# Optimization experiments

Hardware: AMD Instinct MI355X
Metric: run time of the kernel (lower is better)

## Reference

```python
import jax, jax.numpy as jnp
import numpy as np

DIM = 1024
HEADS = 16
SCALE = DIM ** -0.5  # note: source scales by full dim, not head dim


def setup_inputs() -> dict:
    key = jax.random.key(0)
    k1, k2, k3 = jax.random.split(key, 3)
    b, n = 2, 2048
    x = jax.random.normal(k1, (b, n, DIM), dtype=jnp.float32)
    w_qkv = jax.random.normal(k2, (3 * DIM, DIM), dtype=jnp.float32) * (DIM ** -0.5)
    w_out = jax.random.normal(k3, (DIM, DIM), dtype=jnp.float32) * (DIM ** -0.5)
    b_out = jnp.zeros((DIM,), dtype=jnp.float32)
    return {"x": x, "w_qkv": w_qkv, "w_out": w_out, "b_out": b_out}


def reference(x, w_qkv, w_out, b_out):
    b, n, d = x.shape
    h = HEADS
    hd = d // h
    # torch Linear: y = x @ W.T
    qkv = x @ w_qkv.T  # [b, n, 3d]
    q, k, v = jnp.split(qkv, 3, axis=-1)
    # reshape to [b, h, n, hd]
    def to_heads(t):
        return t.reshape(b, n, h, hd).transpose(0, 2, 1, 3)
    q, k, v = to_heads(q), to_heads(k), to_heads(v)
    dots = jnp.einsum('bhqd,bhkd->bhqk', q, k) * SCALE
    attn = jax.nn.softmax(dots, axis=-1)
    out = jnp.einsum('bhqk,bhkd->bhqd', attn, v)
    out = out.transpose(0, 2, 1, 3).reshape(b, n, d)
    return out @ w_out.T + b_out
```

## Files before the change

kernel.cpp:

```cpp
#include <hip/hip_runtime.h>

typedef __attribute__((ext_vector_type(8))) _Float16 half8;
typedef __attribute__((ext_vector_type(4))) _Float16 half4;
typedef __attribute__((ext_vector_type(2))) __fp16 fp16x2;
typedef __attribute__((ext_vector_type(4))) float f32x4;
typedef __attribute__((ext_vector_type(4))) unsigned int u32x4;
typedef __attribute__((ext_vector_type(2))) unsigned int u32x2;

#define NSEQ 2048
#define DIMM 1024
#define NH   16
#define HD   64

typedef const void __attribute__((address_space(1))) gvoid_t;
typedef void __attribute__((address_space(3))) svoid_t;

__device__ __forceinline__ void gload_lds16(const void* g, void* l) {
  __builtin_amdgcn_global_load_lds((gvoid_t*)g, (svoid_t*)l, 16, 0, 0);
}

union H2U { fp16x2 h; unsigned int u; };

__global__ __launch_bounds__(256) void cvt_all(const float* __restrict__ x,
                                               const float* __restrict__ wqkv,
                                               const float* __restrict__ wout,
                                               _Float16* __restrict__ xh,
                                               _Float16* __restrict__ wqkvh,
                                               _Float16* __restrict__ wouth) {
  int i = blockIdx.x * 256 + threadIdx.x;
  const float* src;
  _Float16* dst;
  int off;
  if (i < 524288) { src = x; dst = xh; off = i; }
  else if (i < 917504) { src = wqkv; dst = wqkvh; off = i - 524288; }
  else { src = wout; dst = wouth; off = i - 917504; }
  const float4* p = (const float4*)src + (size_t)off * 2;
  float4 v0 = p[0], v1 = p[1];
  half8 h;
  h[0] = (_Float16)v0.x; h[1] = (_Float16)v0.y; h[2] = (_Float16)v0.z; h[3] = (_Float16)v0.w;
  h[4] = (_Float16)v1.x; h[5] = (_Float16)v1.y; h[6] = (_Float16)v1.z; h[7] = (_Float16)v1.w;
  *((half8*)dst + off) = h;
}

__device__ __forceinline__ void gemm_mainloop(const _Float16* __restrict__ A,
                                              const _Float16* __restrict__ B,
                                              int am0, int bn0,
                                              _Float16* As, _Float16* Bs,
                                              f32x4 acc[4][4]) {
  const int tid = threadIdx.x;
  const int w = tid >> 6, lane = tid & 63;
  const int lr = lane >> 2;
  const int lc = (lane & 3) * 8;
  const int wm = (w >> 1) * 64, wn = (w & 1) * 64;
  const int g = lane >> 4, ln = lane & 15;

  for (int k0 = 0; k0 < 1024; k0 += 32) {
#pragma unroll
    for (int rr = 0; rr < 4; ++rr) {
      int c = rr * 4 + w;
      if (c < 8) {
        gload_lds16(A + (size_t)(am0 + c * 16 + lr) * 1024 + k0 + lc, As + c * 512);
      } else {
        int cb = c - 8;
        gload_lds16(B + (size_t)(bn0 + cb * 16 + lr) * 1024 + k0 + lc, Bs + cb * 512);
      }
    }
    __syncthreads();
    half8 af[4], bf[4];
#pragma unroll
    for (int mi = 0; mi < 4; ++mi)
      af[mi] = *(const half8*)(As + (wm + mi * 16 + ln) * 32 + g * 8);
#pragma unroll
    for (int ni = 0; ni < 4; ++ni)
      bf[ni] = *(const half8*)(Bs + (wn + ni * 16 + ln) * 32 + g * 8);
#pragma unroll
    for (int mi = 0; mi < 4; ++mi)
#pragma unroll
      for (int ni = 0; ni < 4; ++ni)
        acc[mi][ni] = __builtin_amdgcn_mfma_f32_16x16x32_f16(af[mi], bf[ni], acc[mi][ni], 0, 0, 0);
    __syncthreads();
  }
}

union SmemQKV {
  struct { _Float16 a[128 * 32]; _Float16 b[128 * 32]; } ab;
  _Float16 t[128 * 136];
};

#define QSCALE 0.0450843450f

__global__ __launch_bounds__(256) void gemm_qkv(const _Float16* __restrict__ x,
                                                const _Float16* __restrict__ wqkv,
                                                _Float16* __restrict__ qh,
                                                _Float16* __restrict__ kh,
                                                _Float16* __restrict__ vt) {
  __shared__ SmemQKV sh;
  f32x4 acc[4][4];
#pragma unroll
  for (int i = 0; i < 4; ++i)
#pragma unroll
    for (int j = 0; j < 4; ++j) acc[i][j] = (f32x4){0.f, 0.f, 0.f, 0.f};
  const int bm = blockIdx.x, bn = blockIdx.y;
  gemm_mainloop(x, wqkv, bm * 128, bn * 128, sh.ab.a, sh.ab.b, acc);

  const int tid = threadIdx.x;
  const int w = tid >> 6, lane = tid & 63;
  const int g = lane >> 4, ln = lane & 15;
  const int wm = (w >> 1) * 64, wn = (w & 1) * 64;
  const int sec = bn >> 3;
  const int cbase = (bn & 7) * 128;

  if (sec < 2) {
    _Float16* dst = (sec == 0) ? qh : kh;
    const float scale = (sec == 0) ? QSCALE : 1.0f;
#pragma unroll
    for (int mi = 0; mi < 4; ++mi) {
      int row = bm * 128 + wm + mi * 16 + g * 4;
      int bidx = row >> 11, nidx = row & 2047;
#pragma unroll
      for (int ni = 0; ni < 4; ++ni) {
        int col = cbase + wn + ni * 16 + ln;
        int h = col >> 6, d = col & 63;
        _Float16* p = dst + ((size_t)(bidx * NH + h) * NSEQ + nidx) * HD + d;
#pragma unroll
        for (int r = 0; r < 4; ++r) p[r * HD] = (_Float16)(acc[mi][ni][r] * scale);
      }
    }
  } else {
    __syncthreads();
#pragma unroll
    for (int mi = 0; mi < 4; ++mi)
#pragma unroll
      for (int ni = 0; ni < 4; ++ni)
#pragma unroll
        for (int r = 0; r < 4; ++r)
          sh.t[(wn + ni * 16 + ln) * 136 + wm + mi * 16 + g * 4 + r] = (_Float16)acc[mi][ni][r];
    __syncthreads();
    const int row0 = bm * 128;
    const int bidx = row0 >> 11, n0 = row0 & 2047;
#pragma unroll
    for (int i = 0; i < 8; ++i) {
      int ci = i * 256 + tid;
      int drow = ci >> 4, nofs = (ci & 15) * 8;
      int col = cbase + drow;
      int h = col >> 6, d = col & 63;
      u32x4 val = *(const u32x4*)(sh.t + drow * 136 + nofs);
      *(u32x4*)(vt + ((size_t)(bidx * NH + h) * HD + d) * NSEQ + n0 + nofs) = val;
    }
  }
}

__global__ __launch_bounds__(512, 1) void attn_fwd(const _Float16* __restrict__ qg,
                                                   const _Float16* __restrict__ kg,
                                                   const _Float16* __restrict__ vg,
                                                   _Float16* __restrict__ ao) {
  __shared__ _Float16 Ks[2][64 * 64];
  __shared__ _Float16 Vs[2][64 * 64];
  __shared__ _Float16 Ps[8][32 * 64];

  const int bid = blockIdx.x;
  const int swz = (bid & 7) * 32 + (bid >> 3);
  const int bh = swz >> 3, qt = swz & 7;
  const int tid = threadIdx.x, w = tid >> 6, lane = tid & 63;
  const int g = lane >> 4, ln = lane & 15;
  const int sw8 = ln & 7;

  const _Float16* qp = qg + (size_t)bh * NSEQ * HD;
  const _Float16* kp = kg + (size_t)bh * NSEQ * HD;
  const _Float16* vp = vg + (size_t)bh * HD * NSEQ;
  char* psw = (char*)&Ps[w][0];

  const int qr = qt * 256 + w * 32;

  half8 qf[2][2];
#pragma unroll
  for (int qb = 0; qb < 2; ++qb)
#pragma unroll
    for (int dk = 0; dk < 2; ++dk)
      qf[qb][dk] = *(const half8*)(qp + (size_t)(qr + qb * 16 + ln) * HD + dk * 32 + g * 8);
  asm volatile("" ::: "memory");

  const int rsub = lane >> 3;
  const int csw = ((lane & 7) ^ rsub) << 3;

#define STAGE(buf, tt)                                                              \
  {                                                                                 \
    gload_lds16(kp + (size_t)(tt) * 64 * HD + (size_t)(w * 8 + rsub) * HD + csw,    \
                &Ks[buf][w * 512]);                                                 \
    gload_lds16(vp + (size_t)(w * 8 + rsub) * NSEQ + (tt) * 64 + csw,               \
                &Vs[buf][w * 512]);                                                 \
  }

  STAGE(0, 0);

  float lsum[2] = {0.f, 0.f};
  f32x4 oacc[4][2];
#pragma unroll
  for (int sd = 0; sd < 4; ++sd)
#pragma unroll
    for (int qb = 0; qb < 2; ++qb) oacc[sd][qb] = (f32x4){0.f, 0.f, 0.f, 0.f};
  const f32x4 fz = (f32x4){0.f, 0.f, 0.f, 0.f};

#define TILE_BODY(cur)                                                              \
  {                                                                                 \
    f32x4 sacc[4][2];                                                               \
    __builtin_amdgcn_s_setprio(1);                                                  \
    _Pragma("unroll")                                                               \
    for (int s = 0; s < 4; ++s) {                                                   \
      const _Float16* kb = &Ks[cur][(s * 16 + ln) * 64];                            \
      half8 kf0 = *(const half8*)(kb + ((g ^ sw8) << 3));                           \
      half8 kf1 = *(const half8*)(kb + (((4 + g) ^ sw8) << 3));                     \
      sacc[s][0] = __builtin_amdgcn_mfma_f32_16x16x32_f16(kf0, qf[0][0], fz, 0, 0, 0);            \
      sacc[s][0] = __builtin_amdgcn_mfma_f32_16x16x32_f16(kf1, qf[0][1], sacc[s][0], 0, 0, 0);    \
      sacc[s][1] = __builtin_amdgcn_mfma_f32_16x16x32_f16(kf0, qf[1][0], fz, 0, 0, 0);            \
      sacc[s][1] = __builtin_amdgcn_mfma_f32_16x16x32_f16(kf1, qf[1][1], sacc[s][1], 0, 0, 0);    \
    }                                                                               \
    __builtin_amdgcn_s_setprio(0);                                                  \
    _Pragma("unroll")                                                               \
    for (int qb = 0; qb < 2; ++qb) {                                                \
      const int q = qb * 16 + ln;                                                   \
      float rs = 0.f;                                                               \
      _Pragma("unroll")                                                             \
      for (int s = 0; s < 4; ++s) {                                                 \
        float e0 = __builtin_amdgcn_exp2f(sacc[s][qb][0]);                          \
        float e1 = __builtin_amdgcn_exp2f(sacc[s][qb][1]);                          \
        float e2 = __builtin_amdgcn_exp2f(sacc[s][qb][2]);                          \
        float e3 = __builtin_amdgcn_exp2f(sacc[s][qb][3]);                          \
        rs += (e0 + e1) + (e2 + e3);                                                \
        H2U a_, b_;                                                                 \
        a_.h = __builtin_amdgcn_cvt_pkrtz(e0, e1);                                  \
        b_.h = __builtin_amdgcn_cvt_pkrtz(e2, e3);                                  \
        u32x2 quad; quad[0] = a_.u; quad[1] = b_.u;                                 \
        const int kq = s * 4 + g;                                                   \
        *(u32x2*)(psw + q * 128 + ((kq ^ ln) << 3)) = quad;                         \
      }                                                                             \
      lsum[qb] += rs;                                                               \
    }                                                                               \
    asm volatile("s_waitcnt lgkmcnt(0)" ::: "memory");                              \
    half8 pb[2][2];                                                                 \
    _Pragma("unroll")                                                               \
    for (int qb = 0; qb < 2; ++qb) {                                                \
      const int q = qb * 16 + ln;                                                   \
      _Pragma("unroll")                                                             \
      for (int f = 0; f < 2; ++f) {                                                 \
        const int qd = (f * 4 + g) * 2;                                             \
        u32x2 lo = *(const u32x2*)(psw + q * 128 + ((qd ^ ln) << 3));               \
        u32x2 hi = *(const u32x2*)(psw + q * 128 + (((qd + 1) ^ ln) << 3));         \
        union { u32x4 u; half8 h; } pk;                                             \
        pk.u[0] = lo[0]; pk.u[1] = lo[1]; pk.u[2] = hi[0]; pk.u[3] = hi[1];         \
        pb[qb][f] = pk.h;                                                           \
      }                                                                             \
    }                                                                               \
    __builtin_amdgcn_s_setprio(1);                                                  \
    _Pragma("unroll")                                                               \
    for (int sd = 0; sd < 4; ++sd) {                                                \
      const _Float16* vb = &Vs[cur][(sd * 16 + ln) * 64];                           \
      half8 vf0 = *(const half8*)(vb + ((g ^ sw8) << 3));                           \
      half8 vf1 = *(const half8*)(vb + (((4 + g) ^ sw8) << 3));                     \
      _Pragma("unroll")                                                             \
      for (int qb = 0; qb < 2; ++qb) {                                              \
        oacc[sd][qb] = __builtin_amdgcn_mfma_f32_16x16x32_f16(vf0, pb[qb][0], oacc[sd][qb], 0, 0, 0); \
        oacc[sd][qb] = __builtin_amdgcn_mfma_f32_16x16x32_f16(vf1, pb[qb][1], oacc[sd][qb], 0, 0, 0); \
      }                                                                             \
    }                                                                               \
    __builtin_amdgcn_s_setprio(0);                                                  \
  }

  for (int t = 0; t < 31; ++t) {
    const int cur = t & 1;
    STAGE(cur ^ 1, t + 1);
    asm volatile("s_waitcnt vmcnt(2)" ::: "memory");
    __builtin_amdgcn_s_barrier();
    TILE_BODY(cur)
    asm volatile("s_waitcnt lgkmcnt(0)" ::: "memory");
    __builtin_amdgcn_s_barrier();
  }
  {
    asm volatile("s_waitcnt vmcnt(0)" ::: "memory");
    __builtin_amdgcn_s_barrier();
    TILE_BODY(1)
  }

  const int bidx = bh >> 4, h = bh & 15;
#pragma unroll
  for (int qb = 0; qb < 2; ++qb) {
    lsum[qb] += __shfl_xor(lsum[qb], 16, 64);
    lsum[qb] += __shfl_xor(lsum[qb], 32, 64);
    const float inv = 1.f / lsum[qb];
    const int n = qr + qb * 16 + ln;
#pragma unroll
    for (int sd = 0; sd < 4; ++sd) {
      half4 o4;
#pragma unroll
      for (int r = 0; r < 4; ++r) o4[r] = (_Float16)(oacc[sd][qb][r] * inv);
      *(half4*)(ao + (size_t)(bidx * NSEQ + n) * DIMM + h * HD + sd * 16 + g * 4) = o4;
    }
  }
}

__global__ __launch_bounds__(256) void gemm_out(const _Float16* __restrict__ ao,
                                                const _Float16* __restrict__ wout,
                                                const float* __restrict__ bias,
                                                float* __restrict__ out) {
  __shared__ _Float16 As[128 * 32];
  __shared__ _Float16 Bs[128 * 32];
  f32x4 acc[4][4];
#pragma unroll
  for (int i = 0; i < 4; ++i)
#pragma unroll
    for (int j = 0; j < 4; ++j) acc[i][j] = (f32x4){0.f, 0.f, 0.f, 0.f};
  const int bm = blockIdx.x, bn = blockIdx.y;
  gemm_mainloop(ao, wout, bm * 128, bn * 128, As, Bs, acc);
  const int tid = threadIdx.x;
  const int w = tid >> 6, lane = tid & 63;
  const int g = lane >> 4, ln = lane & 15;
  const int wm = (w >> 1) * 64, wn = (w & 1) * 64;
#pragma unroll
  for (int mi = 0; mi < 4; ++mi) {
    const int row = bm * 128 + wm + mi * 16 + g * 4;
#pragma unroll
    for (int ni = 0; ni < 4; ++ni) {
      const int col = bn * 128 + wn + ni * 16 + ln;
      const float b = bias[col];
#pragma unroll
      for (int r = 0; r < 4; ++r) out[(size_t)(row + r) * DIMM + col] = acc[mi][ni][r] + b;
    }
  }
}

extern "C" void kernel_launch(void* const* d_in, const int* in_sizes, int n_in,
                              void* d_out, int out_size, void* d_ws, size_t ws_size,
                              hipStream_t stream) {
  const float* x    = (const float*)d_in[0];
  const float* wqkv = (const float*)d_in[1];
  const float* wout = (const float*)d_in[2];
  const float* bout = (const float*)d_in[3];
  float* out = (float*)d_out;

  _Float16* ws = (_Float16*)d_ws;
  _Float16* x_h    = ws;
  _Float16* wqkv_h = ws + (4u << 20);
  _Float16* wout_h = ws + (7u << 20);
  _Float16* q_h    = ws + (8u << 20);
  _Float16* k_h    = ws + (12u << 20);
  _Float16* vt_h   = ws + (16u << 20);
  _Float16* ao_h   = ws + (20u << 20);

  cvt_all<<<dim3(4096), 256, 0, stream>>>(x, wqkv, wout, x_h, wqkv_h, wout_h);
  gemm_qkv<<<dim3(32, 24), 256, 0, stream>>>(x_h, wqkv_h, q_h, k_h, vt_h);
  attn_fwd<<<dim3(256), 512, 0, stream>>>(q_h, k_h, vt_h, ao_h);
  gemm_out<<<dim3(32, 8), 256, 0, stream>>>(ao_h, wout_h, bout, out);
}
```

Measured before the change: 117.9 us.

## Load K/V tiles directly into registers instead of staging through LDS

The attention kernel no longer stages K and V tiles in shared memory with double buffering and barriers. Each wave now loads its own K and V MFMA fragments straight from global memory into registers, with K prefetched one tile ahead. Blocks shrink to 4 waves and the grid doubles to 512 blocks, with two blocks allowed per CU. This removes LDS traffic and block-wide barriers but makes every wave re-read the full K/V from global memory or L2, and raises register pressure.

```diff
diff --git a/kernel.cpp b/kernel.cpp
--- a/kernel.cpp
+++ b/kernel.cpp
@@ -150,27 +150,24 @@
   }
 }
 
-__global__ __launch_bounds__(512, 1) void attn_fwd(const _Float16* __restrict__ qg,
+__global__ __launch_bounds__(256, 2) void attn_fwd(const _Float16* __restrict__ qg,
                                                    const _Float16* __restrict__ kg,
                                                    const _Float16* __restrict__ vg,
                                                    _Float16* __restrict__ ao) {
-  __shared__ _Float16 Ks[2][64 * 64];
-  __shared__ _Float16 Vs[2][64 * 64];
-  __shared__ _Float16 Ps[8][32 * 64];
+  __shared__ _Float16 Ps[4][32 * 64];
 
   const int bid = blockIdx.x;
-  const int swz = (bid & 7) * 32 + (bid >> 3);
-  const int bh = swz >> 3, qt = swz & 7;
+  const int swz = (bid & 7) * 64 + (bid >> 3);
+  const int bh = swz >> 4, qt = swz & 15;
   const int tid = threadIdx.x, w = tid >> 6, lane = tid & 63;
   const int g = lane >> 4, ln = lane & 15;
-  const int sw8 = ln & 7;
 
   const _Float16* qp = qg + (size_t)bh * NSEQ * HD;
   const _Float16* kp = kg + (size_t)bh * NSEQ * HD;
   const _Float16* vp = vg + (size_t)bh * HD * NSEQ;
   char* psw = (char*)&Ps[w][0];
 
-  const int qr = qt * 256 + w * 32;
+  const int qr = qt * 128 + w * 32;
 
   half8 qf[2][2];
 #pragma unroll
@@ -178,20 +175,26 @@
 #pragma unroll
     for (int dk = 0; dk < 2; ++dk)
       qf[qb][dk] = *(const half8*)(qp + (size_t)(qr + qb * 16 + ln) * HD + dk * 32 + g * 8);
-  asm volatile("" ::: "memory");
-
-  const int rsub = lane >> 3;
-  const int csw = ((lane & 7) ^ rsub) << 3;
-
-#define STAGE(buf, tt)                                                              \
+
+#define LOADK(KR, tt)                                                               \
   {                                                                                 \
-    gload_lds16(kp + (size_t)(tt) * 64 * HD + (size_t)(w * 8 + rsub) * HD + csw,    \
-                &Ks[buf][w * 512]);                                                 \
-    gload_lds16(vp + (size_t)(w * 8 + rsub) * NSEQ + (tt) * 64 + csw,               \
-                &Vs[buf][w * 512]);                                                 \
-  }
-
-  STAGE(0, 0);
+    _Pragma("unroll")                                                               \
+    for (int s = 0; s < 4; ++s) {                                                   \
+      const _Float16* kb_ = kp + (size_t)(((tt) & 31) * 64 + s * 16 + ln) * HD + g * 8; \
+      KR[2 * s]     = *(const half8*)kb_;                                           \
+      KR[2 * s + 1] = *(const half8*)(kb_ + 32);                                    \
+    }                                                                               \
+  }
+
+#define LOADV(VR, tt)                                                               \
+  {                                                                                 \
+    _Pragma("unroll")                                                               \
+    for (int s = 0; s < 4; ++s) {                                                   \
+      const _Float16* vb_ = vp + (size_t)(s * 16 + ln) * NSEQ + ((tt) & 31) * 64 + g * 8; \
+      VR[2 * s]     = *(const half8*)vb_;                                           \
+      VR[2 * s + 1] = *(const half8*)(vb_ + 32);                                    \
+    }                                                                               \
+  }
 
   float lsum[2] = {0.f, 0.f};
   f32x4 oacc[4][2];
@@ -201,19 +204,16 @@
     for (int qb = 0; qb < 2; ++qb) oacc[sd][qb] = (f32x4){0.f, 0.f, 0.f, 0.f};
   const f32x4 fz = (f32x4){0.f, 0.f, 0.f, 0.f};
 
-#define TILE_BODY(cur)                                                              \
+#define TILE(KR, VR)                                                                \
   {                                                                                 \
     f32x4 sacc[4][2];                                                               \
     __builtin_amdgcn_s_setprio(1);                                                  \
     _Pragma("unroll")                                                               \
     for (int s = 0; s < 4; ++s) {                                                   \
-      const _Float16* kb = &Ks[cur][(s * 16 + ln) * 64];                            \
-      half8 kf0 = *(const half8*)(kb + ((g ^ sw8) << 3));                           \
-      half8 kf1 = *(const half8*)(kb + (((4 + g) ^ sw8) << 3));                     \
-      sacc[s][0] = __builtin_amdgcn_mfma_f32_16x16x32_f16(kf0, qf[0][0], fz, 0, 0, 0);            \
-      sacc[s][0] = __builtin_amdgcn_mfma_f32_16x16x32_f16(kf1, qf[0][1], sacc[s][0], 0, 0, 0);    \
-      sacc[s][1] = __builtin_amdgcn_mfma_f32_16x16x32_f16(kf0, qf[1][0], fz, 0, 0, 0);            \
-      sacc[s][1] = __builtin_amdgcn_mfma_f32_16x16x32_f16(kf1, qf[1][1], sacc[s][1], 0, 0, 0);    \
+      sacc[s][0] = __builtin_amdgcn_mfma_f32_16x16x32_f16(KR[2 * s], qf[0][0], fz, 0, 0, 0);            \
+      sacc[s][0] = __builtin_amdgcn_mfma_f32_16x16x32_f16(KR[2 * s + 1], qf[0][1], sacc[s][0], 0, 0, 0);\
+      sacc[s][1] = __builtin_amdgcn_mfma_f32_16x16x32_f16(KR[2 * s], qf[1][0], fz, 0, 0, 0);            \
+      sacc[s][1] = __builtin_amdgcn_mfma_f32_16x16x32_f16(KR[2 * s + 1], qf[1][1], sacc[s][1], 0, 0, 0);\
     }                                                                               \
     __builtin_amdgcn_s_setprio(0);                                                  \
     _Pragma("unroll")                                                               \
@@ -254,31 +254,25 @@
     __builtin_amdgcn_s_setprio(1);                                                  \
     _Pragma("unroll")                                                               \
     for (int sd = 0; sd < 4; ++sd) {                                                \
-      const _Float16* vb = &Vs[cur][(sd * 16 + ln) * 64];                           \
-      half8 vf0 = *(const half8*)(vb + ((g ^ sw8) << 3));                           \
-      half8 vf1 = *(const half8*)(vb + (((4 + g) ^ sw8) << 3));                     \
       _Pragma("unroll")                                                             \
       for (int qb = 0; qb < 2; ++qb) {                                              \
-        oacc[sd][qb] = __builtin_amdgcn_mfma_f32_16x16x32_f16(vf0, pb[qb][0], oacc[sd][qb], 0, 0, 0); \
-        oacc[sd][qb] = __builtin_amdgcn_mfma_f32_16x16x32_f16(vf1, pb[qb][1], oacc[sd][qb], 0, 0, 0); \
+        oacc[sd][qb] = __builtin_amdgcn_mfma_f32_16x16x32_f16(VR[2 * sd], pb[qb][0], oacc[sd][qb], 0, 0, 0);     \
+        oacc[sd][qb] = __builtin_amdgcn_mfma_f32_16x16x32_f16(VR[2 * sd + 1], pb[qb][1], oacc[sd][qb], 0, 0, 0); \
       }                                                                             \
     }                                                                               \
     __builtin_amdgcn_s_setprio(0);                                                  \
   }
 
-  for (int t = 0; t < 31; ++t) {
-    const int cur = t & 1;
-    STAGE(cur ^ 1, t + 1);
-    asm volatile("s_waitcnt vmcnt(2)" ::: "memory");
-    __builtin_amdgcn_s_barrier();
-    TILE_BODY(cur)
-    asm volatile("s_waitcnt lgkmcnt(0)" ::: "memory");
-    __builtin_amdgcn_s_barrier();
-  }
-  {
-    asm volatile("s_waitcnt vmcnt(0)" ::: "memory");
-    __builtin_amdgcn_s_barrier();
-    TILE_BODY(1)
+  half8 kA[8], kB[8], vR[8];
+  LOADK(kA, 0);
+  for (int tt = 0; tt < 16; ++tt) {
+    const int t0 = tt * 2;
+    LOADV(vR, t0);
+    LOADK(kB, t0 + 1);
+    TILE(kA, vR)
+    LOADV(vR, t0 + 1);
+    LOADK(kA, t0 + 2);
+    TILE(kB, vR)
   }
 
   const int bidx = bh >> 4, h = bh & 15;
@@ -348,6 +342,6 @@
 
   cvt_all<<<dim3(4096), 256, 0, stream>>>(x, wqkv, wout, x_h, wqkv_h, wout_h);
   gemm_qkv<<<dim3(32, 24), 256, 0, stream>>>(x_h, wqkv_h, q_h, k_h, vt_h);
-  attn_fwd<<<dim3(256), 512, 0, stream>>>(q_h, k_h, vt_h, ao_h);
+  attn_fwd<<<dim3(512), 256, 0, stream>>>(q_h, k_h, vt_h, ao_h);
   gemm_out<<<dim3(32, 8), 256, 0, stream>>>(ao_h, wout_h, bout, out);
 }
```

After: 184.0 us. 1.56x slower.

## Split attention blocks to 256 threads with triple-buffered K/V staging

Applied to the files above, without the earlier changes.

Attention blocks shrink from 8 waves to 4 waves, each covering 128 query rows, and the grid doubles to 512 blocks so two blocks can share a CU. K/V tiles move to a 3-stage ring buffer with two tiles prefetched ahead. The per-iteration trailing barrier is removed, and V fragments are loaded from LDS before the softmax so their latency overlaps the exp work. Each wave now stages twice as many chunks per tile, and more V fragments stay live in registers, which raises register pressure.

```diff
diff --git a/kernel.cpp b/kernel.cpp
--- a/kernel.cpp
+++ b/kernel.cpp
@@ -150,17 +150,17 @@
   }
 }
 
-__global__ __launch_bounds__(512, 1) void attn_fwd(const _Float16* __restrict__ qg,
+__global__ __launch_bounds__(256, 2) void attn_fwd(const _Float16* __restrict__ qg,
                                                    const _Float16* __restrict__ kg,
                                                    const _Float16* __restrict__ vg,
                                                    _Float16* __restrict__ ao) {
-  __shared__ _Float16 Ks[2][64 * 64];
-  __shared__ _Float16 Vs[2][64 * 64];
-  __shared__ _Float16 Ps[8][32 * 64];
+  __shared__ _Float16 Ks[3][64 * 64];
+  __shared__ _Float16 Vs[3][64 * 64];
+  __shared__ _Float16 Ps[4][32 * 64];
 
   const int bid = blockIdx.x;
-  const int swz = (bid & 7) * 32 + (bid >> 3);
-  const int bh = swz >> 3, qt = swz & 7;
+  const int swz = (bid & 7) * 64 + (bid >> 3);
+  const int bh = swz >> 4, qt = swz & 15;
   const int tid = threadIdx.x, w = tid >> 6, lane = tid & 63;
   const int g = lane >> 4, ln = lane & 15;
   const int sw8 = ln & 7;
@@ -170,7 +170,7 @@
   const _Float16* vp = vg + (size_t)bh * HD * NSEQ;
   char* psw = (char*)&Ps[w][0];
 
-  const int qr = qt * 256 + w * 32;
+  const int qr = qt * 128 + w * 32;
 
   half8 qf[2][2];
 #pragma unroll
@@ -182,16 +182,26 @@
 
   const int rsub = lane >> 3;
   const int csw = ((lane & 7) ^ rsub) << 3;
+  const int c0 = 2 * w;
 
 #define STAGE(buf, tt)                                                              \
   {                                                                                 \
-    gload_lds16(kp + (size_t)(tt) * 64 * HD + (size_t)(w * 8 + rsub) * HD + csw,    \
-                &Ks[buf][w * 512]);                                                 \
-    gload_lds16(vp + (size_t)(w * 8 + rsub) * NSEQ + (tt) * 64 + csw,               \
-                &Vs[buf][w * 512]);                                                 \
+    const _Float16* kt_ = kp + (size_t)(tt) * 64 * HD;                              \
+    _Pragma("unroll")                                                               \
+    for (int i = 0; i < 2; ++i) {                                                   \
+      int c = c0 + i;                                                               \
+      gload_lds16(kt_ + (size_t)(c * 8 + rsub) * HD + csw, &Ks[buf][c * 512]);      \
+    }                                                                               \
+    _Pragma("unroll")                                                               \
+    for (int i = 0; i < 2; ++i) {                                                   \
+      int c = c0 + i;                                                               \
+      gload_lds16(vp + (size_t)(c * 8 + rsub) * NSEQ + (tt) * 64 + csw,             \
+                  &Vs[buf][c * 512]);                                               \
+    }                                                                               \
   }
 
   STAGE(0, 0);
+  STAGE(1, 1);
 
   float lsum[2] = {0.f, 0.f};
   f32x4 oacc[4][2];
@@ -201,21 +211,30 @@
     for (int qb = 0; qb < 2; ++qb) oacc[sd][qb] = (f32x4){0.f, 0.f, 0.f, 0.f};
   const f32x4 fz = (f32x4){0.f, 0.f, 0.f, 0.f};
 
-#define TILE_BODY(cur)                                                              \
+#define TILE_BODY(kbuf, vbuf)                                                       \
   {                                                                                 \
+    const _Float16* kb_ = (kbuf);                                                   \
+    const _Float16* vb_ = (vbuf);                                                   \
     f32x4 sacc[4][2];                                                               \
     __builtin_amdgcn_s_setprio(1);                                                  \
     _Pragma("unroll")                                                               \
     for (int s = 0; s < 4; ++s) {                                                   \
-      const _Float16* kb = &Ks[cur][(s * 16 + ln) * 64];                            \
-      half8 kf0 = *(const half8*)(kb + ((g ^ sw8) << 3));                           \
-      half8 kf1 = *(const half8*)(kb + (((4 + g) ^ sw8) << 3));                     \
+      const _Float16* kr = kb_ + (s * 16 + ln) * 64;                                \
+      half8 kf0 = *(const half8*)(kr + ((g ^ sw8) << 3));                           \
+      half8 kf1 = *(const half8*)(kr + (((4 + g) ^ sw8) << 3));                     \
       sacc[s][0] = __builtin_amdgcn_mfma_f32_16x16x32_f16(kf0, qf[0][0], fz, 0, 0, 0);            \
       sacc[s][0] = __builtin_amdgcn_mfma_f32_16x16x32_f16(kf1, qf[0][1], sacc[s][0], 0, 0, 0);    \
       sacc[s][1] = __builtin_amdgcn_mfma_f32_16x16x32_f16(kf0, qf[1][0], fz, 0, 0, 0);            \
       sacc[s][1] = __builtin_amdgcn_mfma_f32_16x16x32_f16(kf1, qf[1][1], sacc[s][1], 0, 0, 0);    \
     }                                                                               \
     __builtin_amdgcn_s_setprio(0);                                                  \
+    half8 vf[4][2];           \
+    _Pragma("unroll")                                                               \
+    for (int sd = 0; sd < 4; ++sd) {                                                \
+      const _Float16* vr = vb_ + (sd * 16 + ln) * 64;                               \
+      vf[sd][0] = *(const half8*)(vr + ((g ^ sw8) << 3));                           \
+      vf[sd][1] = *(const half8*)(vr + (((4 + g) ^ sw8) << 3));                     \
+    }                                                                               \
     _Pragma("unroll")                                                               \
     for (int qb = 0; qb < 2; ++qb) {                                                \
       const int q = qb * 16 + ln;                                                   \
@@ -236,7 +255,7 @@
       }                                                                             \
       lsum[qb] += rs;                                                               \
     }                                                                               \
-    asm volatile("s_waitcnt lgkmcnt(0)" ::: "memory");                              \
+    asm volatile("s_waitcnt lgkmcnt(0)" ::: "memory");  \
     half8 pb[2][2];                                                                 \
     _Pragma("unroll")                                                               \
     for (int qb = 0; qb < 2; ++qb) {                                                \
@@ -254,31 +273,30 @@
     __builtin_amdgcn_s_setprio(1);                                                  \
     _Pragma("unroll")                                                               \
     for (int sd = 0; sd < 4; ++sd) {                                                \
-      const _Float16* vb = &Vs[cur][(sd * 16 + ln) * 64];                           \
-      half8 vf0 = *(const half8*)(vb + ((g ^ sw8) << 3));                           \
-      half8 vf1 = *(const half8*)(vb + (((4 + g) ^ sw8) << 3));                     \
       _Pragma("unroll")                                                             \
       for (int qb = 0; qb < 2; ++qb) {                                              \
-        oacc[sd][qb] = __builtin_amdgcn_mfma_f32_16x16x32_f16(vf0, pb[qb][0], oacc[sd][qb], 0, 0, 0); \
-        oacc[sd][qb] = __builtin_amdgcn_mfma_f32_16x16x32_f16(vf1, pb[qb][1], oacc[sd][qb], 0, 0, 0); \
+        oacc[sd][qb] = __builtin_amdgcn_mfma_f32_16x16x32_f16(vf[sd][0], pb[qb][0], oacc[sd][qb], 0, 0, 0); \
+        oacc[sd][qb] = __builtin_amdgcn_mfma_f32_16x16x32_f16(vf[sd][1], pb[qb][1], oacc[sd][qb], 0, 0, 0); \
       }                                                                             \
     }                                                                               \
     __builtin_amdgcn_s_setprio(0);                                                  \
   }
 
-  for (int t = 0; t < 31; ++t) {
-    const int cur = t & 1;
-    STAGE(cur ^ 1, t + 1);
-    asm volatile("s_waitcnt vmcnt(2)" ::: "memory");
+  for (int t = 0; t < 30; ++t) {
+    asm volatile("s_waitcnt vmcnt(4)" ::: "memory");
     __builtin_amdgcn_s_barrier();
-    TILE_BODY(cur)
-    asm volatile("s_waitcnt lgkmcnt(0)" ::: "memory");
+    STAGE((t + 2) % 3, t + 2);
+    TILE_BODY(&Ks[t % 3][0], &Vs[t % 3][0])
+  }
+  {
+    asm volatile("s_waitcnt vmcnt(4)" ::: "memory");
     __builtin_amdgcn_s_barrier();
+    TILE_BODY(&Ks[0][0], &Vs[0][0])
   }
   {
     asm volatile("s_waitcnt vmcnt(0)" ::: "memory");
     __builtin_amdgcn_s_barrier();
-    TILE_BODY(1)
+    TILE_BODY(&Ks[1][0], &Vs[1][0])
   }
 
   const int bidx = bh >> 4, h = bh & 15;
@@ -348,6 +366,6 @@
 
   cvt_all<<<dim3(4096), 256, 0, stream>>>(x, wqkv, wout, x_h, wqkv_h, wout_h);
   gemm_qkv<<<dim3(32, 24), 256, 0, stream>>>(x_h, wqkv_h, q_h, k_h, vt_h);
-  attn_fwd<<<dim3(256), 512, 0, stream>>>(q_h, k_h, vt_h, ao_h);
+  attn_fwd<<<dim3(512), 256, 0, stream>>>(q_h, k_h, vt_h, ao_h);
   gemm_out<<<dim3(32, 8), 256, 0, stream>>>(ao_h, wout_h, bout, out);
 }
```

Result: faster. 115.4 us (-2.1%).
